# Kernel optimization log

Hardware: AMD Instinct MI355X
Metric: run time of the kernel (lower is better)

## Reference

```python
import jax, jax.numpy as jnp
import numpy as np

ALPHA = 0.85  # de-emphasis coefficient (module default)


def setup_inputs() -> dict:
    key = jax.random.key(0)
    signal = jax.random.normal(key, (64, 960000), dtype=jnp.float32)
    return {"signal": signal}


def reference(signal):
    # y[n] = x[n] + alpha * y[n-1]  (zero initial state), i.e.
    # lfilter([1], [1, -alpha], signal) along the last axis.
    # Expressed as a parallel associative scan over affine maps
    # y -> a*y + b with per-step element (a, b) = (alpha, x[n]).
    def combine(e1, e2):
        a1, b1 = e1
        a2, b2 = e2
        return (a1 * a2, a2 * b1 + b2)

    a = jnp.full_like(signal, ALPHA)
    _, y = jax.lax.associative_scan(combine, (a, signal), axis=-1)
    return y
```

## Files before the change

### kernel.cpp

```cpp
#include <hip/hip_runtime.h>


#define ALPHA 0.85f

constexpr int ROW    = 960000;
constexpr int T      = 16;
constexpr int BT     = 256;
constexpr int TOT    = T * BT;
constexpr int LOOK   = 256;
constexpr int CHUNK  = TOT - LOOK;
constexpr int CHUNKS = ROW / CHUNK;

constexpr float apow(int n) {
    double r = 1.0;
    for (int i = 0; i < n; ++i) r *= 0.85;
    return (float)r;
}

constexpr float A16   = apow(16);
constexpr float A32   = apow(32);
constexpr float A64   = apow(64);
constexpr float A128  = apow(128);
constexpr float A256  = apow(256);
constexpr float A512  = apow(512);
constexpr float A1024 = apow(1024);
constexpr float LOG2_A16 = -3.7514440648f;

__global__ __launch_bounds__(BT) void deemph_kernel(const float* __restrict__ x,
                                                    float* __restrict__ y) {
    const int blk = blockIdx.x;
    const int r   = blk / CHUNKS;
    const int c   = blk - r * CHUNKS;
    const int t   = threadIdx.x;

    const long long rowbase = (long long)r * ROW;
    const long long inbase = rowbase + (long long)c * CHUNK - LOOK + (long long)t * T;

    float v[T];
    if (c == 0 && t < LOOK / T) {
        #pragma unroll
        for (int i = 0; i < T; ++i) v[i] = 0.0f;
    } else {
        const float4* p = (const float4*)(x + inbase);
        #pragma unroll
        for (int i = 0; i < T / 4; ++i) {
            float4 q = p[i];
            v[4*i+0] = q.x; v[4*i+1] = q.y; v[4*i+2] = q.z; v[4*i+3] = q.w;
        }
    }

    float s = 0.0f;
    #pragma unroll
    for (int i = 0; i < T; ++i) { s = v[i] + ALPHA * s; v[i] = s; }

    const int lane = t & 63;
    float acc = s;
    {
        float up;
        up = __shfl_up(acc, 1, 64);  if (lane >= 1)  acc += A16  * up;
        up = __shfl_up(acc, 2, 64);  if (lane >= 2)  acc += A32  * up;
        up = __shfl_up(acc, 4, 64);  if (lane >= 4)  acc += A64  * up;
        up = __shfl_up(acc, 8, 64);  if (lane >= 8)  acc += A128 * up;
        up = __shfl_up(acc, 16, 64); if (lane >= 16) acc += A256 * up;
        up = __shfl_up(acc, 32, 64); if (lane >= 32) acc += A512 * up;
    }

    __shared__ float wsum[BT / 64];
    const int wave = t >> 6;
    if (lane == 63) wsum[wave] = acc;
    __syncthreads();
    float W = 0.0f;
    for (int w2 = 0; w2 < wave; ++w2) W = wsum[w2] + A1024 * W;

    float excl = __shfl_up(acc, 1, 64);
    if (lane == 0) excl = 0.0f;
    const float P = excl + exp2f((float)lane * LOG2_A16) * W;

    if (t >= LOOK / T) {
        float m = ALPHA;
        float o[T];
        #pragma unroll
        for (int i = 0; i < T; ++i) { o[i] = v[i] + m * P; m *= ALPHA; }
        float4* q = (float4*)(y + inbase);
        #pragma unroll
        for (int i = 0; i < T / 4; ++i) {
            float4 w4 = { o[4*i+0], o[4*i+1], o[4*i+2], o[4*i+3] };
            q[i] = w4;
        }
    }
}

extern "C" void kernel_launch(void* const* d_in, const int* in_sizes, int n_in,
                              void* d_out, int out_size, void* d_ws, size_t ws_size,
                              hipStream_t stream) {
    const float* x = (const float*)d_in[0];
    float* y = (float*)d_out;
    const int nrows = in_sizes[0] / ROW;
    deemph_kernel<<<dim3(nrows * CHUNKS), dim3(BT), 0, stream>>>(x, y);
}
```

Before: 403.8 us.

## Stage loads and stores through padded LDS for coalesced global access

```diff
diff --git a/kernel.cpp b/kernel.cpp
--- a/kernel.cpp
+++ b/kernel.cpp
@@ -2,6 +2,8 @@
 
 
 #define ALPHA 0.85f
+
+typedef float vf4 __attribute__((ext_vector_type(4)));
 
 constexpr int ROW    = 960000;
 constexpr int T      = 16;
@@ -10,6 +12,7 @@
 constexpr int LOOK   = 256;
 constexpr int CHUNK  = TOT - LOOK;
 constexpr int CHUNKS = ROW / CHUNK;
+constexpr int LSTRIDE = 20;
 
 constexpr float apow(int n) {
     double r = 1.0;
@@ -28,25 +31,36 @@
 
 __global__ __launch_bounds__(BT) void deemph_kernel(const float* __restrict__ x,
                                                     float* __restrict__ y) {
+    __shared__ float lds[BT * LSTRIDE];
+
     const int blk = blockIdx.x;
     const int r   = blk / CHUNKS;
     const int c   = blk - r * CHUNKS;
     const int t   = threadIdx.x;
 
     const long long rowbase = (long long)r * ROW;
-    const long long inbase = rowbase + (long long)c * CHUNK - LOOK + (long long)t * T;
+    const long long win0    = rowbase + (long long)c * CHUNK - LOOK;
+
+    #pragma unroll
+    for (int k = 0; k < 4; ++k) {
+        const int p4 = t + BT * k;
+        const int e  = p4 << 2;
+        vf4 q;
+        if (c == 0 && e < LOOK) {
+            q = (vf4){0.f, 0.f, 0.f, 0.f};
+        } else {
+            q = *(const vf4*)(x + win0 + e);
+        }
+        const int owner = e >> 4, off = e & 15;
+        *(vf4*)&lds[owner * LSTRIDE + off] = q;
+    }
+    __syncthreads();
 
     float v[T];
-    if (c == 0 && t < LOOK / T) {
-        #pragma unroll
-        for (int i = 0; i < T; ++i) v[i] = 0.0f;
-    } else {
-        const float4* p = (const float4*)(x + inbase);
-        #pragma unroll
-        for (int i = 0; i < T / 4; ++i) {
-            float4 q = p[i];
-            v[4*i+0] = q.x; v[4*i+1] = q.y; v[4*i+2] = q.z; v[4*i+3] = q.w;
-        }
+    #pragma unroll
+    for (int j = 0; j < T / 4; ++j) {
+        vf4 q = *(const vf4*)&lds[t * LSTRIDE + 4 * j];
+        v[4*j+0] = q.x; v[4*j+1] = q.y; v[4*j+2] = q.z; v[4*j+3] = q.w;
     }
 
     float s = 0.0f;
@@ -76,16 +90,29 @@
     if (lane == 0) excl = 0.0f;
     const float P = excl + exp2f((float)lane * LOG2_A16) * W;
 
-    if (t >= LOOK / T) {
+    {
         float m = ALPHA;
-        float o[T];
         #pragma unroll
-        for (int i = 0; i < T; ++i) { o[i] = v[i] + m * P; m *= ALPHA; }
-        float4* q = (float4*)(y + inbase);
-        #pragma unroll
-        for (int i = 0; i < T / 4; ++i) {
-            float4 w4 = { o[4*i+0], o[4*i+1], o[4*i+2], o[4*i+3] };
-            q[i] = w4;
+        for (int j = 0; j < T / 4; ++j) {
+            vf4 q;
+            q.x = v[4*j+0] + m * P; m *= ALPHA;
+            q.y = v[4*j+1] + m * P; m *= ALPHA;
+            q.z = v[4*j+2] + m * P; m *= ALPHA;
+            q.w = v[4*j+3] + m * P; m *= ALPHA;
+            *(vf4*)&lds[t * LSTRIDE + 4 * j] = q;
+        }
+    }
+    __syncthreads();
+
+    const long long outbase = rowbase + (long long)c * CHUNK;
+    #pragma unroll
+    for (int k = 0; k < 4; ++k) {
+        const int p4 = t + BT * k;
+        if (p4 < CHUNK / 4) {
+            const int e = LOOK + (p4 << 2);
+            const int owner = e >> 4, off = e & 15;
+            const vf4 q = *(const vf4*)&lds[owner * LSTRIDE + off];
+            __builtin_nontemporal_store(q, (vf4*)(y + outbase + (p4 << 2)));
         }
     }
 }
```

Measured after the change: 406.4 us. No clear change (+0.7%).
